# Kernel optimization log

Measured on AMD Instinct MI355X. Metric: run time of the kernel, lower is better.

## Reference

```python
import jax, jax.numpy as jnp
import numpy as np

N = 20000          # nodes
E = 200000         # edges
IN = 256           # in_channels
OUT = 256          # out_channels (heads * per-head)
H = 2              # heads
C = OUT // 2       # per-head channels (out_channels // 2)
TDIM = 100         # time_enc.out_channels
MSG = 156          # msg_dim
EDGE_DIM = TDIM + MSG  # 256
P = 0.1            # dropout prob


def setup_inputs() -> dict:
    key = jax.random.key(0)
    ks = jax.random.split(key, 20)
    s = 1.0 / np.sqrt(IN)
    se = 1.0 / np.sqrt(EDGE_DIM)
    return {
        "x": jax.random.normal(ks[0], (N, IN), jnp.float32),
        "last_update": jax.random.uniform(ks[1], (N,), jnp.float32) * 100.0,
        "edge_index": jax.random.randint(ks[2], (2, E), 0, N, jnp.int64),
        "t": jax.random.uniform(ks[3], (E,), jnp.float32) * 100.0,
        "msg": jax.random.normal(ks[4], (E, MSG), jnp.float32),
        "u_edge": jax.random.uniform(ks[5], (E,), jnp.float32),
        "u_attn": jax.random.uniform(ks[6], (E, H), jnp.float32),
        # TimeEncoder: cos(Linear(1, TDIM))
        "time_w": jax.random.normal(ks[7], (TDIM,), jnp.float32),
        "time_b": jax.random.normal(ks[8], (TDIM,), jnp.float32) * 0.1,
        # TransformerConv params ([in, out] layout)
        "Wq": jax.random.normal(ks[9], (IN, H * C), jnp.float32) * s,
        "bq": jnp.zeros((H * C,), jnp.float32),
        "Wk": jax.random.normal(ks[10], (IN, H * C), jnp.float32) * s,
        "bk": jnp.zeros((H * C,), jnp.float32),
        "Wv": jax.random.normal(ks[11], (IN, H * C), jnp.float32) * s,
        "bv": jnp.zeros((H * C,), jnp.float32),
        "We": jax.random.normal(ks[12], (EDGE_DIM, H * C), jnp.float32) * se,
        "be": jnp.zeros((H * C,), jnp.float32),
        "Ws": jax.random.normal(ks[13], (IN, H * C), jnp.float32) * s,
        "bs": jnp.zeros((H * C,), jnp.float32),
    }


def reference(x, last_update, edge_index, t, msg, u_edge, u_attn,
              time_w, time_b, Wq, bq, Wk, bk, Wv, bv, We, be, Ws, bs):
    src, dst = edge_index[0], edge_index[1]
    # time encoding of relative time (TGN TimeEncoder: cos(Linear(1, TDIM)))
    rel_t = last_update[src] - t                              # [E]
    rel_enc = jnp.cos(rel_t[:, None] * time_w[None, :] + time_b)  # [E, TDIM]
    edge_attr = jnp.concatenate([rel_enc, msg], axis=-1)      # [E, EDGE_DIM]
    # dropout_adj: drop edges with prob P (no rescale)
    keep = u_edge > P                                         # [E] bool

    q = (x @ Wq + bq).reshape(N, H, C)
    k = (x @ Wk + bk).reshape(N, H, C)
    v = (x @ Wv + bv).reshape(N, H, C)
    e = (edge_attr @ We + be).reshape(E, H, C)

    kj = k[src] + e                                           # [E, H, C]
    alpha = jnp.einsum('ehc,ehc->eh', q[dst], kj) / jnp.sqrt(jnp.float32(C))
    alpha = jnp.where(keep[:, None], alpha, -jnp.inf)
    # segment softmax over incoming edges of each dst node
    m = jax.ops.segment_max(alpha, dst, num_segments=N)       # [N, H]
    m = jnp.where(jnp.isfinite(m), m, 0.0)
    ex = jnp.where(keep[:, None], jnp.exp(alpha - m[dst]), 0.0)
    denom = jax.ops.segment_sum(ex, dst, num_segments=N)      # [N, H]
    attn = ex / (denom[dst] + 1e-16)                          # [E, H]
    # attention dropout (post-softmax, inverted scaling)
    attn = attn * (u_attn > P).astype(attn.dtype) / (1.0 - P)

    msg_out = (v[src] + e) * attn[:, :, None]                 # [E, H, C]
    out = jax.ops.segment_sum(msg_out, dst, num_segments=N).reshape(N, H * C)
    # root/skip connection
    return out + (x @ Ws + bs)
```

## Files before the change

### kernel.cpp

```cpp
#include <hip/hip_runtime.h>

#define NND 20000
#define NE 200000
#define PDROP 0.1f

typedef unsigned short u16;
typedef __bf16 bf16x8 __attribute__((ext_vector_type(8)));
typedef float f32x4 __attribute__((ext_vector_type(4)));

__device__ __forceinline__ float b2f(u16 u) {
  unsigned v = ((unsigned)u) << 16;
  float f;
  __builtin_memcpy(&f, &v, 4);
  return f;
}
__device__ __forceinline__ u16 f2b(float f) {
  unsigned x;
  __builtin_memcpy(&x, &f, 4);
  unsigned r = x + 0x7fffu + ((x >> 16) & 1u);
  return (u16)(r >> 16);
}

__global__ void convert_x(const float* __restrict__ x, u16* __restrict__ xb) {
  int i = blockIdx.x * blockDim.x + threadIdx.x;
  if (i < NND * 256 / 4) {
    float4 v = ((const float4*)x)[i];
    ushort4 o;
    o.x = f2b(v.x); o.y = f2b(v.y); o.z = f2b(v.z); o.w = f2b(v.w);
    ((ushort4*)xb)[i] = o;
  }
}

struct WTArgs {
  const float* W[6];
  u16* WT[6];
};
__global__ void convert_wT(WTArgs a) {
  int gid = blockIdx.x * blockDim.x + threadIdx.x;
  if (gid >= 6 * 65536) return;
  int w = gid >> 16, r = gid & 65535;
  if (w < 5) {
    int n = r >> 8, k = r & 255;
    a.WT[w][n * 256 + k] = f2b(a.W[w][k * 256 + n]);
  } else {
    a.WT[5][r] = f2b(a.W[5][r]);
  }
}

__global__ void zero2(int* __restrict__ cnt, int* __restrict__ cur) {
  int i = blockIdx.x * blockDim.x + threadIdx.x;
  if (i < NND) { cnt[i] = 0; cur[i] = 0; }
}
__global__ void csr_count(const int* __restrict__ ei, int* __restrict__ cnt) {
  int e = blockIdx.x * blockDim.x + threadIdx.x;
  if (e < NE) atomicAdd(&cnt[ei[NE + e]], 1);
}
__global__ __launch_bounds__(1024) void scan_rowptr(const int* __restrict__ cnt,
                                                    int* __restrict__ rowptr) {
  __shared__ int sums[1024];
  const int tid = threadIdx.x;
  const int base = tid * 20;
  int local[20];
  int run = 0;
#pragma unroll
  for (int i = 0; i < 20; i++) {
    int idx = base + i;
    local[i] = run;
    run += (idx < NND) ? cnt[idx] : 0;
  }
  sums[tid] = run;
  __syncthreads();
  for (int off = 1; off < 1024; off <<= 1) {
    int v = (tid >= off) ? sums[tid - off] : 0;
    __syncthreads();
    sums[tid] += v;
    __syncthreads();
  }
  int prev = (tid > 0) ? sums[tid - 1] : 0;
#pragma unroll
  for (int i = 0; i < 20; i++) {
    int idx = base + i;
    if (idx < NND) rowptr[idx] = prev + local[i];
  }
  if (tid == 1023) rowptr[NND] = sums[1023];
}
__global__ void csr_fill(const int* __restrict__ ei,
                         const float* __restrict__ last_update,
                         const float* __restrict__ t,
                         const float* __restrict__ u_edge,
                         const float* __restrict__ u_attn,
                         const int* __restrict__ rowptr, int* __restrict__ cur,
                         int* __restrict__ elist, uint4* __restrict__ recs) {
  int e = blockIdx.x * blockDim.x + threadIdx.x;
  if (e < NE) {
    int s = ei[e];
    int d = ei[NE + e];
    int p = rowptr[d] + atomicAdd(&cur[d], 1);
    elist[p] = e;
    bool keep = u_edge[e] > PDROP;
    float rt = last_update[s] - t[e];
    float2 ua = *(const float2*)&u_attn[(size_t)e * 2];
    uint4 r;
    r.x = (unsigned)s | (keep ? 0u : 0x80000000u);
    r.y = __float_as_uint(rt);
    r.z = __float_as_uint(ua.x > PDROP ? (1.f / 0.9f) : 0.f);
    r.w = __float_as_uint(ua.y > PDROP ? (1.f / 0.9f) : 0.f);
    recs[p] = r;
  }
}

__device__ __forceinline__ void mfma_tile(const u16 (*As)[72], const u16 (*Bs)[72],
                                          f32x4 acc[4][4], int wm, int wn,
                                          int fr, int fg) {
#pragma unroll
  for (int ks = 0; ks < 2; ks++) {
    bf16x8 a[4], b[4];
#pragma unroll
    for (int i = 0; i < 4; i++)
      a[i] = *(const bf16x8*)&As[wm * 64 + i * 16 + fr][ks * 32 + fg * 8];
#pragma unroll
    for (int j = 0; j < 4; j++)
      b[j] = *(const bf16x8*)&Bs[wn * 64 + j * 16 + fr][ks * 32 + fg * 8];
#pragma unroll
    for (int i = 0; i < 4; i++)
#pragma unroll
      for (int j = 0; j < 4; j++)
        acc[i][j] = __builtin_amdgcn_mfma_f32_16x16x32_bf16(a[i], b[j], acc[i][j], 0, 0, 0);
  }
}

struct NodeArgs {
  const u16* BT[4];
  const float* bias[4];
  u16* outb[3];
  float* outf;
};
__global__ __launch_bounds__(256) void gemm_node(const u16* __restrict__ xb,
                                                 NodeArgs args) {
  __shared__ __attribute__((aligned(16))) u16 As[128][72];
  __shared__ __attribute__((aligned(16))) u16 Bs[128][72];
  const int tid = threadIdx.x;
  const int w = blockIdx.y >> 1;
  const int col0 = (blockIdx.y & 1) * 128;
  const int row0 = blockIdx.x * 128;
  const u16* BT = args.BT[w];
  const float* bias = args.bias[w];
  const int wid = tid >> 6, lane = tid & 63;
  const int wm = wid >> 1, wn = wid & 1;
  const int fr = lane & 15, fg = lane >> 4;
  f32x4 acc[4][4] = {};
  for (int k0 = 0; k0 < 256; k0 += 64) {
#pragma unroll
    for (int i = 0; i < 4; i++) {
      int idx = tid + i * 256;
      int row = idx >> 3, vc = idx & 7;
      int g = row0 + row;
      uint4 v = make_uint4(0, 0, 0, 0);
      if (g < NND) v = *(const uint4*)&xb[(size_t)g * 256 + k0 + vc * 8];
      *(uint4*)&As[row][vc * 8] = v;
      *(uint4*)&Bs[row][vc * 8] = *(const uint4*)&BT[(size_t)(col0 + row) * 256 + k0 + vc * 8];
    }
    __syncthreads();
    mfma_tile(As, Bs, acc, wm, wn, fr, fg);
    __syncthreads();
  }
#pragma unroll
  for (int mi = 0; mi < 4; mi++) {
#pragma unroll
    for (int rr = 0; rr < 4; rr++) {
      int grow = row0 + wm * 64 + mi * 16 + fg * 4 + rr;
      if (grow >= NND) continue;
#pragma unroll
      for (int ni = 0; ni < 4; ni++) {
        int gcol = col0 + wn * 64 + ni * 16 + fr;
        float val = acc[mi][ni][rr] + bias[gcol];
        if (w < 3)
          args.outb[w][(size_t)grow * 256 + gcol] = f2b(val);
        else
          args.outf[(size_t)grow * 256 + gcol] = val;
      }
    }
  }
}

__global__ __launch_bounds__(256) void gemm_qwe(const u16* __restrict__ qb,
                                                const u16* __restrict__ Web,
                                                u16* __restrict__ qWeb) {
  __shared__ __attribute__((aligned(16))) u16 As[128][72];
  __shared__ __attribute__((aligned(16))) u16 Bs[128][72];
  const int tid = threadIdx.x;
  const int h = blockIdx.y >> 1;
  const int col0 = (blockIdx.y & 1) * 128;
  const int row0 = blockIdx.x * 128;
  const int wid = tid >> 6, lane = tid & 63;
  const int wm = wid >> 1, wn = wid & 1;
  const int fr = lane & 15, fg = lane >> 4;
  f32x4 acc[4][4] = {};
  for (int k0 = 0; k0 < 128; k0 += 64) {
#pragma unroll
    for (int i = 0; i < 4; i++) {
      int idx = tid + i * 256;
      int row = idx >> 3, vc = idx & 7;
      int g = row0 + row;
      uint4 v = make_uint4(0, 0, 0, 0);
      if (g < NND) v = *(const uint4*)&qb[(size_t)g * 256 + h * 128 + k0 + vc * 8];
      *(uint4*)&As[row][vc * 8] = v;
      *(uint4*)&Bs[row][vc * 8] =
          *(const uint4*)&Web[(size_t)(col0 + row) * 256 + h * 128 + k0 + vc * 8];
    }
    __syncthreads();
    mfma_tile(As, Bs, acc, wm, wn, fr, fg);
    __syncthreads();
  }
#pragma unroll
  for (int mi = 0; mi < 4; mi++) {
#pragma unroll
    for (int rr = 0; rr < 4; rr++) {
      int grow = row0 + wm * 64 + mi * 16 + fg * 4 + rr;
      if (grow >= NND) continue;
#pragma unroll
      for (int ni = 0; ni < 4; ni++) {
        int gj = col0 + wn * 64 + ni * 16 + fr;
        qWeb[(size_t)grow * 512 + h * 256 + gj] = f2b(acc[mi][ni][rr]);
      }
    }
  }
}

__global__ __launch_bounds__(256) void node_fused(
    const u16* __restrict__ qb, const u16* __restrict__ kb,
    const u16* __restrict__ vb, const u16* __restrict__ qWeb,
    const float* __restrict__ msg, const float* __restrict__ tw,
    const float* __restrict__ tb_, const float* __restrict__ be,
    const int* __restrict__ rowptr, const int* __restrict__ elist,
    const uint4* __restrict__ recs, u16* __restrict__ aggb,
    float* __restrict__ out) {
  const int node = (blockIdx.x * blockDim.x + threadIdx.x) >> 6;
  const int lane = threadIdx.x & 63;
  if (node >= NND) return;
  const int beg = rowptr[node], end = rowptr[node + 1];
  const int c0 = lane * 4, hl = lane >> 5;

  ushort4 q4 = *(const ushort4*)&qb[(size_t)node * 256 + c0];
  float qf0 = b2f(q4.x), qf1 = b2f(q4.y), qf2 = b2f(q4.z), qf3 = b2f(q4.w);
  ushort4 w0v = *(const ushort4*)&qWeb[(size_t)node * 512 + c0];
  ushort4 w1v = *(const ushort4*)&qWeb[(size_t)node * 512 + 256 + c0];
  float qw00 = b2f(w0v.x), qw01 = b2f(w0v.y), qw02 = b2f(w0v.z), qw03 = b2f(w0v.w);
  float qw10 = b2f(w1v.x), qw11 = b2f(w1v.y), qw12 = b2f(w1v.z), qw13 = b2f(w1v.w);
  float4 bev = *(const float4*)&be[c0];
  float pb = qf0 * bev.x + qf1 * bev.y + qf2 * bev.z + qf3 * bev.w;
#pragma unroll
  for (int off = 16; off; off >>= 1) pb += __shfl_xor(pb, off);
  float tw0 = 0, tw1 = 0, tw2 = 0, tw3 = 0, tb0 = 0, tb1 = 0, tb2 = 0, tb3 = 0;
  if (c0 < 100) {
    float4 a = *(const float4*)&tw[c0];
    float4 b = *(const float4*)&tb_[c0];
    tw0 = a.x; tw1 = a.y; tw2 = a.z; tw3 = a.w;
    tb0 = b.x; tb1 = b.y; tb2 = b.z; tb3 = b.w;
  }
  const float inv = 0.08838834764831845f;

  float m0 = -INFINITY, m1 = -INFINITY;
  float den0 = 0.f, den1 = 0.f, sw0 = 0.f, sw1 = 0.f;
  float vc0 = 0, vc1 = 0, vc2 = 0, vc3 = 0;
  float g00 = 0, g01 = 0, g02 = 0, g03 = 0;
  float g10 = 0, g11 = 0, g12 = 0, g13 = 0;

  unsigned seC = 0; float rtC = 0, wk0C = 0, wk1C = 0;
  ushort4 k4C = make_ushort4(0, 0, 0, 0), v4C = make_ushort4(0, 0, 0, 0);
  float4 mmC = make_float4(0, 0, 0, 0);

#define LOAD_SLOT(J, se, rt, w0_, w1_, k4, v4, mm)                        \
  {                                                                       \
    uint4 rr_ = recs[J];                                                  \
    se = rr_.x; rt = __uint_as_float(rr_.y);                              \
    w0_ = __uint_as_float(rr_.z); w1_ = __uint_as_float(rr_.w);           \
    int s_ = (int)(se & 0x7fffffffu);                                     \
    k4 = *(const ushort4*)&kb[(size_t)s_ * 256 + c0];                     \
    v4 = *(const ushort4*)&vb[(size_t)s_ * 256 + c0];                     \
    if (c0 >= 100) {                                                      \
      int eid_ = elist[J];                                                \
      mm = *(const float4*)&msg[(size_t)eid_ * 156 + (c0 - 100)];         \
    }                                                                     \
  }

  if (beg < end) LOAD_SLOT(beg, seC, rtC, wk0C, wk1C, k4C, v4C, mmC);

  for (int j = beg; j < end; ++j) {
    unsigned seN = 0; float rtN = 0, wk0N = 0, wk1N = 0;
    ushort4 k4N = make_ushort4(0, 0, 0, 0), v4N = make_ushort4(0, 0, 0, 0);
    float4 mmN = make_float4(0, 0, 0, 0);
    if (j + 1 < end) LOAD_SLOT(j + 1, seN, rtN, wk0N, wk1N, k4N, v4N, mmN);

    float ea0, ea1, ea2, ea3;
    if (c0 < 100) {
      ea0 = __cosf(rtC * tw0 + tb0); ea1 = __cosf(rtC * tw1 + tb1);
      ea2 = __cosf(rtC * tw2 + tb2); ea3 = __cosf(rtC * tw3 + tb3);
    } else {
      ea0 = mmC.x; ea1 = mmC.y; ea2 = mmC.z; ea3 = mmC.w;
    }
    float pqk = qf0 * b2f(k4C.x) + qf1 * b2f(k4C.y) +
                qf2 * b2f(k4C.z) + qf3 * b2f(k4C.w);
    float pe0 = qw00 * ea0 + qw01 * ea1 + qw02 * ea2 + qw03 * ea3;
    float pe1 = qw10 * ea0 + qw11 * ea1 + qw12 * ea2 + qw13 * ea3;
    float y0 = pe0 + __shfl_xor(pe0, 32);
    float y1 = pe1 + __shfl_xor(pe1, 32);
    float z = (lane < 32) ? y0 : y1;
#pragma unroll
    for (int off = 16; off; off >>= 1) {
      z += __shfl_xor(z, off);
      pqk += __shfl_xor(pqk, off);
    }
    float a = (seC < 0x80000000u) ? (pqk + z + pb) * inv : -INFINITY;
    float aoth = __shfl_xor(a, 32);
    float a0 = (lane < 32) ? a : aoth;
    float a1 = (lane < 32) ? aoth : a;
    if (a0 > m0) {
      float sc = (m0 > -1e30f) ? __expf(m0 - a0) : 0.f;
      den0 *= sc; sw0 *= sc;
      g00 *= sc; g01 *= sc; g02 *= sc; g03 *= sc;
      float scv = hl ? 1.f : sc;
      vc0 *= scv; vc1 *= scv; vc2 *= scv; vc3 *= scv;
      m0 = a0;
    }
    if (a1 > m1) {
      float sc = (m1 > -1e30f) ? __expf(m1 - a1) : 0.f;
      den1 *= sc; sw1 *= sc;
      g10 *= sc; g11 *= sc; g12 *= sc; g13 *= sc;
      float scv = hl ? sc : 1.f;
      vc0 *= scv; vc1 *= scv; vc2 *= scv; vc3 *= scv;
      m1 = a1;
    }
    float ex0 = (a0 > -1e30f) ? __expf(a0 - m0) : 0.f;
    float ex1 = (a1 > -1e30f) ? __expf(a1 - m1) : 0.f;
    den0 += ex0; den1 += ex1;
    float w0 = ex0 * wk0C;
    float w1 = ex1 * wk1C;
    float wv = hl ? w1 : w0;
    vc0 += wv * b2f(v4C.x); vc1 += wv * b2f(v4C.y);
    vc2 += wv * b2f(v4C.z); vc3 += wv * b2f(v4C.w);
    g00 += w0 * ea0; g01 += w0 * ea1; g02 += w0 * ea2; g03 += w0 * ea3;
    g10 += w1 * ea0; g11 += w1 * ea1; g12 += w1 * ea2; g13 += w1 * ea3;
    sw0 += w0; sw1 += w1;

    seC = seN; rtC = rtN; wk0C = wk0N; wk1C = wk1N;
    k4C = k4N; v4C = v4N; mmC = mmN;
  }
#undef LOAD_SLOT

  float rden0 = 1.f / (den0 + 1e-16f), rden1 = 1.f / (den1 + 1e-16f);
  float rv = hl ? rden1 : rden0;
  float swv = hl ? sw1 : sw0;
  float4 o = *(float4*)&out[(size_t)node * 256 + c0];
  o.x += (vc0 + swv * bev.x) * rv;
  o.y += (vc1 + swv * bev.y) * rv;
  o.z += (vc2 + swv * bev.z) * rv;
  o.w += (vc3 + swv * bev.w) * rv;
  *(float4*)&out[(size_t)node * 256 + c0] = o;
  ushort4 a0v, a1v;
  a0v.x = f2b(g00 * rden0); a0v.y = f2b(g01 * rden0);
  a0v.z = f2b(g02 * rden0); a0v.w = f2b(g03 * rden0);
  a1v.x = f2b(g10 * rden1); a1v.y = f2b(g11 * rden1);
  a1v.z = f2b(g12 * rden1); a1v.w = f2b(g13 * rden1);
  *(ushort4*)&aggb[(size_t)node * 256 + c0] = a0v;
  *(ushort4*)&aggb[(size_t)(NND + node) * 256 + c0] = a1v;
}

__global__ __launch_bounds__(256) void gemm_final(const u16* __restrict__ aggb,
                                                  const u16* __restrict__ WeT,
                                                  float* __restrict__ out) {
  __shared__ __attribute__((aligned(16))) u16 As[128][72];
  __shared__ __attribute__((aligned(16))) u16 Bs[128][72];
  const int tid = threadIdx.x;
  const int h = blockIdx.y;
  const int row0 = blockIdx.x * 128;
  const u16* A = aggb + (size_t)h * NND * 256;
  const int wid = tid >> 6, lane = tid & 63;
  const int wm = wid >> 1, wn = wid & 1;
  const int fr = lane & 15, fg = lane >> 4;
  f32x4 acc[4][4] = {};
  for (int k0 = 0; k0 < 256; k0 += 64) {
#pragma unroll
    for (int i = 0; i < 4; i++) {
      int idx = tid + i * 256;
      int row = idx >> 3, vc = idx & 7;
      int g = row0 + row;
      uint4 v = make_uint4(0, 0, 0, 0);
      if (g < NND) v = *(const uint4*)&A[(size_t)g * 256 + k0 + vc * 8];
      *(uint4*)&As[row][vc * 8] = v;
      *(uint4*)&Bs[row][vc * 8] =
          *(const uint4*)&WeT[(size_t)(h * 128 + row) * 256 + k0 + vc * 8];
    }
    __syncthreads();
    mfma_tile(As, Bs, acc, wm, wn, fr, fg);
    __syncthreads();
  }
#pragma unroll
  for (int mi = 0; mi < 4; mi++) {
#pragma unroll
    for (int rr = 0; rr < 4; rr++) {
      int grow = row0 + wm * 64 + mi * 16 + fg * 4 + rr;
      if (grow >= NND) continue;
#pragma unroll
      for (int ni = 0; ni < 4; ni++) {
        int gcol = wn * 64 + ni * 16 + fr;
        out[(size_t)grow * 256 + h * 128 + gcol] += acc[mi][ni][rr];
      }
    }
  }
}

extern "C" void kernel_launch(void* const* d_in, const int* in_sizes, int n_in,
                              void* d_out, int out_size, void* d_ws, size_t ws_size,
                              hipStream_t stream) {
  const float* x = (const float*)d_in[0];
  const float* last_update = (const float*)d_in[1];
  const int* ei = (const int*)d_in[2];
  const float* t = (const float*)d_in[3];
  const float* msg = (const float*)d_in[4];
  const float* u_edge = (const float*)d_in[5];
  const float* u_attn = (const float*)d_in[6];
  const float* time_w = (const float*)d_in[7];
  const float* time_b = (const float*)d_in[8];
  const float* Wq = (const float*)d_in[9];
  const float* bq = (const float*)d_in[10];
  const float* Wk = (const float*)d_in[11];
  const float* bk = (const float*)d_in[12];
  const float* Wv = (const float*)d_in[13];
  const float* bv = (const float*)d_in[14];
  const float* We = (const float*)d_in[15];
  const float* be = (const float*)d_in[16];
  const float* Ws = (const float*)d_in[17];
  const float* bs = (const float*)d_in[18];
  float* out = (float*)d_out;

  char* ws = (char*)d_ws;
  u16* xb = (u16*)(ws + 0);
  u16* WT0 = (u16*)(ws + 10240000);
  u16* qb = (u16*)(ws + 11026432);
  u16* kb = (u16*)(ws + 21266432);
  u16* vb = (u16*)(ws + 31506432);
  u16* qWeb = (u16*)(ws + 41746432);
  u16* aggb = (u16*)(ws + 62226432);
  uint4* recs = (uint4*)(ws + 82706432);
  int* cnt = (int*)(ws + 85906432);
  int* cur = (int*)(ws + 85986432);
  int* rowptr = (int*)(ws + 86066432);
  int* elist = (int*)(ws + 86146448);

  zero2<<<(NND + 255) / 256, 256, 0, stream>>>(cnt, cur);
  csr_count<<<(NE + 255) / 256, 256, 0, stream>>>(ei, cnt);
  scan_rowptr<<<1, 1024, 0, stream>>>(cnt, rowptr);
  csr_fill<<<(NE + 255) / 256, 256, 0, stream>>>(ei, last_update, t, u_edge,
                                                 u_attn, rowptr, cur, elist,
                                                 recs);

  WTArgs wa;
  wa.W[0] = Wq; wa.W[1] = Wk; wa.W[2] = Wv; wa.W[3] = Ws; wa.W[4] = We; wa.W[5] = We;
  for (int i = 0; i < 6; i++) wa.WT[i] = WT0 + (size_t)i * 65536;
  convert_wT<<<(6 * 65536 + 255) / 256, 256, 0, stream>>>(wa);
  convert_x<<<(NND * 64 + 255) / 256, 256, 0, stream>>>(x, xb);

  NodeArgs na;
  na.BT[0] = wa.WT[0]; na.BT[1] = wa.WT[1]; na.BT[2] = wa.WT[2]; na.BT[3] = wa.WT[3];
  na.bias[0] = bq; na.bias[1] = bk; na.bias[2] = bv; na.bias[3] = bs;
  na.outb[0] = qb; na.outb[1] = kb; na.outb[2] = vb;
  na.outf = out;
  dim3 gn((NND + 127) / 128, 8);
  gemm_node<<<gn, 256, 0, stream>>>(xb, na);

  dim3 gq((NND + 127) / 128, 4);
  gemm_qwe<<<gq, 256, 0, stream>>>(qb, wa.WT[5], qWeb);

  node_fused<<<(NND + 3) / 4, 256, 0, stream>>>(
      qb, kb, vb, qWeb, msg, time_w, time_b, be, rowptr, elist, recs, aggb,
      out);

  dim3 gf((NND + 127) / 128, 2);
  gemm_final<<<gf, 256, 0, stream>>>(aggb, wa.WT[4], out);
}
```

Measured before the change: 264.4 us.

## Process incoming edges in batches of four in fused attention-aggregate loop

Replaces the one-edge software-pipelined loop in the per-node online softmax aggregation with a loop that handles four edges per step. All gathers for four edges are issued together, the shuffle reductions are interleaved across the four, and the running max is updated once per batch instead of once per edge. This raises memory-level parallelism and instruction-level parallelism, and cuts rescale branches. The cost is higher register pressure and padded work on tail batches for low-degree nodes.

```diff
diff --git a/kernel.cpp b/kernel.cpp
--- a/kernel.cpp
+++ b/kernel.cpp
@@ -266,87 +266,99 @@
   float g00 = 0, g01 = 0, g02 = 0, g03 = 0;
   float g10 = 0, g11 = 0, g12 = 0, g13 = 0;
 
-  unsigned seC = 0; float rtC = 0, wk0C = 0, wk1C = 0;
-  ushort4 k4C = make_ushort4(0, 0, 0, 0), v4C = make_ushort4(0, 0, 0, 0);
-  float4 mmC = make_float4(0, 0, 0, 0);
-
-#define LOAD_SLOT(J, se, rt, w0_, w1_, k4, v4, mm)                        \
-  {                                                                       \
-    uint4 rr_ = recs[J];                                                  \
-    se = rr_.x; rt = __uint_as_float(rr_.y);                              \
-    w0_ = __uint_as_float(rr_.z); w1_ = __uint_as_float(rr_.w);           \
-    int s_ = (int)(se & 0x7fffffffu);                                     \
-    k4 = *(const ushort4*)&kb[(size_t)s_ * 256 + c0];                     \
-    v4 = *(const ushort4*)&vb[(size_t)s_ * 256 + c0];                     \
-    if (c0 >= 100) {                                                      \
-      int eid_ = elist[J];                                                \
-      mm = *(const float4*)&msg[(size_t)eid_ * 156 + (c0 - 100)];         \
-    }                                                                     \
-  }
-
-  if (beg < end) LOAD_SLOT(beg, seC, rtC, wk0C, wk1C, k4C, v4C, mmC);
-
-  for (int j = beg; j < end; ++j) {
-    unsigned seN = 0; float rtN = 0, wk0N = 0, wk1N = 0;
-    ushort4 k4N = make_ushort4(0, 0, 0, 0), v4N = make_ushort4(0, 0, 0, 0);
-    float4 mmN = make_float4(0, 0, 0, 0);
-    if (j + 1 < end) LOAD_SLOT(j + 1, seN, rtN, wk0N, wk1N, k4N, v4N, mmN);
-
-    float ea0, ea1, ea2, ea3;
+  for (int j0 = beg; j0 < end; j0 += 4) {
+    float ea[4][4];
+    unsigned se[4];
+    float rt[4], wk0[4], wk1[4];
+    ushort4 k4[4], v4[4];
+#pragma unroll
+    for (int e = 0; e < 4; ++e) {
+      int j = j0 + e;
+      int jc = (j < end) ? j : (end - 1);
+      uint4 rr = recs[jc];
+      bool valid = (j < end);
+      se[e] = valid ? rr.x : 0xFFFFFFFFu;
+      rt[e] = __uint_as_float(rr.y);
+      wk0[e] = valid ? __uint_as_float(rr.z) : 0.f;
+      wk1[e] = valid ? __uint_as_float(rr.w) : 0.f;
+      int s_ = (int)(rr.x & 0x7fffffffu);
+      k4[e] = *(const ushort4*)&kb[(size_t)s_ * 256 + c0];
+      v4[e] = *(const ushort4*)&vb[(size_t)s_ * 256 + c0];
+      if (c0 >= 100) {
+        int eid = elist[jc];
+        *(float4*)&ea[e][0] = *(const float4*)&msg[(size_t)eid * 156 + (c0 - 100)];
+      }
+    }
     if (c0 < 100) {
-      ea0 = __cosf(rtC * tw0 + tb0); ea1 = __cosf(rtC * tw1 + tb1);
-      ea2 = __cosf(rtC * tw2 + tb2); ea3 = __cosf(rtC * tw3 + tb3);
-    } else {
-      ea0 = mmC.x; ea1 = mmC.y; ea2 = mmC.z; ea3 = mmC.w;
-    }
-    float pqk = qf0 * b2f(k4C.x) + qf1 * b2f(k4C.y) +
-                qf2 * b2f(k4C.z) + qf3 * b2f(k4C.w);
-    float pe0 = qw00 * ea0 + qw01 * ea1 + qw02 * ea2 + qw03 * ea3;
-    float pe1 = qw10 * ea0 + qw11 * ea1 + qw12 * ea2 + qw13 * ea3;
-    float y0 = pe0 + __shfl_xor(pe0, 32);
-    float y1 = pe1 + __shfl_xor(pe1, 32);
-    float z = (lane < 32) ? y0 : y1;
+#pragma unroll
+      for (int e = 0; e < 4; ++e) {
+        ea[e][0] = __cosf(rt[e] * tw0 + tb0);
+        ea[e][1] = __cosf(rt[e] * tw1 + tb1);
+        ea[e][2] = __cosf(rt[e] * tw2 + tb2);
+        ea[e][3] = __cosf(rt[e] * tw3 + tb3);
+      }
+    }
+    float z[4], pq[4];
+#pragma unroll
+    for (int e = 0; e < 4; ++e) {
+      pq[e] = qf0 * b2f(k4[e].x) + qf1 * b2f(k4[e].y) +
+              qf2 * b2f(k4[e].z) + qf3 * b2f(k4[e].w);
+      float pe0 = qw00 * ea[e][0] + qw01 * ea[e][1] + qw02 * ea[e][2] + qw03 * ea[e][3];
+      float pe1 = qw10 * ea[e][0] + qw11 * ea[e][1] + qw12 * ea[e][2] + qw13 * ea[e][3];
+      float y0 = pe0 + __shfl_xor(pe0, 32);
+      float y1 = pe1 + __shfl_xor(pe1, 32);
+      z[e] = (lane < 32) ? y0 : y1;
+    }
 #pragma unroll
     for (int off = 16; off; off >>= 1) {
-      z += __shfl_xor(z, off);
-      pqk += __shfl_xor(pqk, off);
-    }
-    float a = (seC < 0x80000000u) ? (pqk + z + pb) * inv : -INFINITY;
-    float aoth = __shfl_xor(a, 32);
-    float a0 = (lane < 32) ? a : aoth;
-    float a1 = (lane < 32) ? aoth : a;
-    if (a0 > m0) {
-      float sc = (m0 > -1e30f) ? __expf(m0 - a0) : 0.f;
+#pragma unroll
+      for (int e = 0; e < 4; ++e) {
+        z[e] += __shfl_xor(z[e], off);
+        pq[e] += __shfl_xor(pq[e], off);
+      }
+    }
+    float a0[4], a1[4];
+#pragma unroll
+    for (int e = 0; e < 4; ++e) {
+      float a = (se[e] < 0x80000000u) ? (pq[e] + z[e] + pb) * inv : -INFINITY;
+      float aoth = __shfl_xor(a, 32);
+      a0[e] = (lane < 32) ? a : aoth;
+      a1[e] = (lane < 32) ? aoth : a;
+    }
+    float cm0 = fmaxf(fmaxf(a0[0], a0[1]), fmaxf(a0[2], a0[3]));
+    float cm1 = fmaxf(fmaxf(a1[0], a1[1]), fmaxf(a1[2], a1[3]));
+    if (cm0 > m0) {
+      float sc = (m0 > -1e30f) ? __expf(m0 - cm0) : 0.f;
       den0 *= sc; sw0 *= sc;
       g00 *= sc; g01 *= sc; g02 *= sc; g03 *= sc;
       float scv = hl ? 1.f : sc;
       vc0 *= scv; vc1 *= scv; vc2 *= scv; vc3 *= scv;
-      m0 = a0;
-    }
-    if (a1 > m1) {
-      float sc = (m1 > -1e30f) ? __expf(m1 - a1) : 0.f;
+      m0 = cm0;
+    }
+    if (cm1 > m1) {
+      float sc = (m1 > -1e30f) ? __expf(m1 - cm1) : 0.f;
       den1 *= sc; sw1 *= sc;
       g10 *= sc; g11 *= sc; g12 *= sc; g13 *= sc;
       float scv = hl ? sc : 1.f;
       vc0 *= scv; vc1 *= scv; vc2 *= scv; vc3 *= scv;
-      m1 = a1;
-    }
-    float ex0 = (a0 > -1e30f) ? __expf(a0 - m0) : 0.f;
-    float ex1 = (a1 > -1e30f) ? __expf(a1 - m1) : 0.f;
-    den0 += ex0; den1 += ex1;
-    float w0 = ex0 * wk0C;
-    float w1 = ex1 * wk1C;
-    float wv = hl ? w1 : w0;
-    vc0 += wv * b2f(v4C.x); vc1 += wv * b2f(v4C.y);
-    vc2 += wv * b2f(v4C.z); vc3 += wv * b2f(v4C.w);
-    g00 += w0 * ea0; g01 += w0 * ea1; g02 += w0 * ea2; g03 += w0 * ea3;
-    g10 += w1 * ea0; g11 += w1 * ea1; g12 += w1 * ea2; g13 += w1 * ea3;
-    sw0 += w0; sw1 += w1;
-
-    seC = seN; rtC = rtN; wk0C = wk0N; wk1C = wk1N;
-    k4C = k4N; v4C = v4N; mmC = mmN;
-  }
-#undef LOAD_SLOT
+      m1 = cm1;
+    }
+#pragma unroll
+    for (int e = 0; e < 4; ++e) {
+      float ex0 = (a0[e] > -1e30f) ? __expf(a0[e] - m0) : 0.f;
+      float ex1 = (a1[e] > -1e30f) ? __expf(a1[e] - m1) : 0.f;
+      den0 += ex0; den1 += ex1;
+      float w0 = ex0 * wk0[e], w1 = ex1 * wk1[e];
+      float wv = hl ? w1 : w0;
+      vc0 += wv * b2f(v4[e].x); vc1 += wv * b2f(v4[e].y);
+      vc2 += wv * b2f(v4[e].z); vc3 += wv * b2f(v4[e].w);
+      g00 += w0 * ea[e][0]; g01 += w0 * ea[e][1];
+      g02 += w0 * ea[e][2]; g03 += w0 * ea[e][3];
+      g10 += w1 * ea[e][0]; g11 += w1 * ea[e][1];
+      g12 += w1 * ea[e][2]; g13 += w1 * ea[e][3];
+      sw0 += w0; sw1 += w1;
+    }
+  }
 
   float rden0 = 1.f / (den0 + 1e-16f), rden1 = 1.f / (den1 + 1e-16f);
   float rv = hl ? rden1 : rden0;
```

Measured after the change: 249.1 us. 5.8% less time.
